# Kernel tuning notes

Hardware: AMD Instinct MI355X
Metric: run time of the kernel (lower is better)

The kernel has to match this reference:

```python
import jax, jax.numpy as jnp
import numpy as np

D = 1024
H = 16
DH = D // H


def setup_inputs() -> dict:
    key = jax.random.key(0)
    ks = jax.random.split(key, 11)
    B, T = 4, 2048
    s = 0.02
    return {
        "q": jax.random.normal(ks[0], (B, T, D), jnp.float32),
        "k": jax.random.normal(ks[1], (B, T, D), jnp.float32),
        "v": jax.random.normal(ks[2], (B, T, D), jnp.float32),
        "Wq": jax.random.normal(ks[3], (D, D), jnp.float32) * s,
        "b_q": jax.random.normal(ks[4], (D,), jnp.float32) * s,
        "Wk": jax.random.normal(ks[5], (D, D), jnp.float32) * s,
        "b_k": jax.random.normal(ks[6], (D,), jnp.float32) * s,
        "Wv": jax.random.normal(ks[7], (D, D), jnp.float32) * s,
        "b_v": jax.random.normal(ks[8], (D,), jnp.float32) * s,
        "Wo": jax.random.normal(ks[9], (D, D), jnp.float32) * s,
        "b_o": jax.random.normal(ks[10], (D,), jnp.float32) * s,
    }


def reference(q, k, v, Wq, b_q, Wk, b_k, Wv, b_v, Wo, b_o):
    B, Tq, _ = q.shape
    Tk = k.shape[1]
    # linear projections, split heads: [B,T,H,DH]
    Q = (q @ Wq + b_q).reshape(B, Tq, H, DH)
    K = (k @ Wk + b_k).reshape(B, Tk, H, DH)
    V = (v @ Wv + b_v).reshape(B, Tk, H, DH)
    # scaled dot-product attention (scale by sqrt(dh), matching q.shape[-1])
    scores = jnp.einsum('bthd,bshd->bhts', Q, K) / jnp.sqrt(jnp.float32(DH))
    P = jax.nn.softmax(scores, axis=-1)  # [B,H,Tq,Tk]
    out = jnp.einsum('bhts,bshd->bthd', P, V).reshape(B, Tq, D)
    return out @ Wo + b_o
```

## Files before the change

kernel.cpp:

```cpp
#include <hip/hip_runtime.h>
#include <hip/hip_bf16.h>


typedef __attribute__((ext_vector_type(8))) short bf16x8;
typedef __attribute__((ext_vector_type(4))) float f32x4;
typedef __attribute__((ext_vector_type(16))) float f32x16;

constexpr int Bc  = 4;
constexpr int Tc  = 2048;
constexpr int Dc  = 1024;
constexpr int Hc  = 16;
constexpr int DHc = 64;
constexpr int Mc  = Bc * Tc;

#define DI __device__ __forceinline__
#define MFMA32 __builtin_amdgcn_mfma_f32_32x32x16_bf16

DI void gload_lds16(const void* g, void* lds) {
  __builtin_amdgcn_global_load_lds((const __attribute__((address_space(1))) void*)g,
                                   (__attribute__((address_space(3))) void*)lds, 16, 0, 0);
}

DI uint pkbf(float lo, float hi) {
  union { __hip_bfloat16 h[2]; uint u; } t;
  t.h[0] = __float2bfloat16(lo);
  t.h[1] = __float2bfloat16(hi);
  return t.u;
}

DI f32x16 zero16() {
  f32x16 z;
#pragma unroll
  for (int i = 0; i < 16; ++i) z[i] = 0.f;
  return z;
}

__global__ __launch_bounds__(256) void cvt_f32_bf16(const float* __restrict__ in,
                                                    __hip_bfloat16* __restrict__ out,
                                                    int n8) {
  int i = blockIdx.x * 256 + threadIdx.x;
  if (i >= n8) return;
  float4 a = ((const float4*)in)[(size_t)i * 2];
  float4 b = ((const float4*)in)[(size_t)i * 2 + 1];
  alignas(16) __hip_bfloat16 t[8];
  t[0] = __float2bfloat16(a.x); t[1] = __float2bfloat16(a.y);
  t[2] = __float2bfloat16(a.z); t[3] = __float2bfloat16(a.w);
  t[4] = __float2bfloat16(b.x); t[5] = __float2bfloat16(b.y);
  t[6] = __float2bfloat16(b.z); t[7] = __float2bfloat16(b.w);
  *(uint4*)(out + (size_t)i * 8) = *(const uint4*)t;
}

__global__ __launch_bounds__(256) void wtrans(const float* __restrict__ W,
                                              __hip_bfloat16* __restrict__ Wt) {
  __shared__ __hip_bfloat16 tile[32][33];
  int n0 = blockIdx.x * 32, k0 = blockIdx.y * 32;
  int tx = threadIdx.x, ty = threadIdx.y;
#pragma unroll
  for (int i = 0; i < 4; ++i) {
    int k = ty + i * 8;
    tile[k][tx] = __float2bfloat16(W[(size_t)(k0 + k) * Dc + n0 + tx]);
  }
  __syncthreads();
#pragma unroll
  for (int i = 0; i < 4; ++i) {
    int n = ty + i * 8;
    Wt[(size_t)(n0 + n) * Dc + k0 + tx] = tile[tx][n];
  }
}

__global__ __launch_bounds__(256) void vtrans(const __hip_bfloat16* __restrict__ Vn,
                                              __hip_bfloat16* __restrict__ Vt) {
  __shared__ __hip_bfloat16 tile[64][72];
  int t0 = blockIdx.x * 64, h = blockIdx.y, b = blockIdx.z;
  int tid = threadIdx.x;
  int r = tid >> 3, ch = tid & 7;
#pragma unroll
  for (int half = 0; half < 2; ++half) {
    int row = r + half * 32;
    *(bf16x8*)&tile[row][ch * 8] =
        *(const bf16x8*)(Vn + ((size_t)(b * Tc + t0 + row)) * Dc + h * DHc + ch * 8);
  }
  __syncthreads();
#pragma unroll
  for (int half = 0; half < 2; ++half) {
    int dh = r + half * 32;
    bf16x8 v;
#pragma unroll
    for (int j = 0; j < 8; ++j) v[j] = *(const short*)&tile[ch * 8 + j][dh];
    *(bf16x8*)(Vt + ((size_t)((b * Hc + h) * DHc + dh)) * Tc + t0 + ch * 8) = v;
  }
}

template <bool OUT_BF16>
__global__ __launch_bounds__(256) void gemm_bt(const __hip_bfloat16* __restrict__ A,
                                               const __hip_bfloat16* __restrict__ Bt,
                                               const float* __restrict__ bias,
                                               void* __restrict__ Cout,
                                               int M, int N, int Kd, float scale) {
  constexpr int BK = 32;
  __shared__ __hip_bfloat16 Alds[128][BK];
  __shared__ __hip_bfloat16 Blds[128][BK];
  int tid = threadIdx.x;
  int w = tid >> 6, l = tid & 63;
  int lr = l & 15, lh = l >> 4;
  int wr = w >> 1, wc = w & 1;

  int g = blockIdx.y * gridDim.x + blockIdx.x;
  int nwg = gridDim.x * gridDim.y;
  int swz = ((g & 7) * (nwg >> 3)) + (g >> 3);
  int nbx = gridDim.x;
  int bx = swz % nbx, by = swz / nbx;
  int brow = by * 128, bcol = bx * 128;

  f32x4 acc[4][4];
#pragma unroll
  for (int mi = 0; mi < 4; ++mi)
#pragma unroll
    for (int ni = 0; ni < 4; ++ni) acc[mi][ni] = (f32x4){0.f, 0.f, 0.f, 0.f};

  int srow_in_ch = l >> 2;
  int scol = (l & 3) * 8;

  const int nkt = Kd / BK;
  for (int kt = 0; kt < nkt; ++kt) {
#pragma unroll
    for (int c = 0; c < 2; ++c) {
      int wch = w * 2 + c;
      int row = wch * 16 + srow_in_ch;
      const __hip_bfloat16* ga = A  + ((size_t)(brow + row)) * Kd + kt * BK + scol;
      const __hip_bfloat16* gb = Bt + ((size_t)(bcol + row)) * Kd + kt * BK + scol;
      gload_lds16(ga, (char*)&Alds[0][0] + wch * 1024);
      gload_lds16(gb, (char*)&Blds[0][0] + wch * 1024);
    }
    __syncthreads();
    bf16x8 af[4], bfr[4];
#pragma unroll
    for (int mi = 0; mi < 4; ++mi)
      af[mi] = *(const bf16x8*)&Alds[wr * 64 + mi * 16 + lr][lh * 8];
#pragma unroll
    for (int ni = 0; ni < 4; ++ni)
      bfr[ni] = *(const bf16x8*)&Blds[wc * 64 + ni * 16 + lr][lh * 8];
#pragma unroll
    for (int mi = 0; mi < 4; ++mi)
#pragma unroll
      for (int ni = 0; ni < 4; ++ni)
        acc[mi][ni] = __builtin_amdgcn_mfma_f32_16x16x32_bf16(af[mi], bfr[ni], acc[mi][ni], 0, 0, 0);
    __syncthreads();
  }

#pragma unroll
  for (int mi = 0; mi < 4; ++mi)
#pragma unroll
    for (int ni = 0; ni < 4; ++ni) {
      int row = brow + wr * 64 + mi * 16 + lh * 4;
      int col = bcol + wc * 64 + ni * 16 + lr;
      float bv = bias[col];
#pragma unroll
      for (int i = 0; i < 4; ++i) {
        float v = (acc[mi][ni][i] + bv) * scale;
        if (OUT_BF16)
          ((__hip_bfloat16*)Cout)[(size_t)(row + i) * N + col] = __float2bfloat16(v);
        else
          ((float*)Cout)[(size_t)(row + i) * N + col] = v;
      }
    }
}

__global__ __launch_bounds__(256, 2) void attn(const __hip_bfloat16* __restrict__ Q,
                                               const __hip_bfloat16* __restrict__ K,
                                               const __hip_bfloat16* __restrict__ Vt,
                                               __hip_bfloat16* __restrict__ O) {
  __shared__ __hip_bfloat16 Kl[2][64][64];
  __shared__ __hip_bfloat16 Vl[2][64][64];

  int g = blockIdx.x;
  int swz = (g & 7) * 128 + (g >> 3);
  int qt = swz & 15, h = (swz >> 4) & 15, b = swz >> 8;

  int tid = threadIdx.x, w = tid >> 6, l = tid & 63;
  int lane31 = l & 31, hi = l >> 5;
  int s7 = lane31 & 7;

  const __hip_bfloat16* qp =
      Q + ((size_t)(b * Tc + qt * 128 + w * 32 + lane31)) * Dc + h * DHc;
  bf16x8 qa[4];
#pragma unroll
  for (int c = 0; c < 4; ++c) qa[c] = *(const bf16x8*)(qp + c * 16 + hi * 8);

  int srow0 = w * 8 + (l >> 3);
  int srow1 = srow0 + 32;
  int sch0 = (l & 7) ^ (srow0 & 7);
  int sch1 = (l & 7) ^ (srow1 & 7);
  const __hip_bfloat16* kg0 = K + ((size_t)(b * Tc + srow0)) * Dc + h * DHc + sch0 * 8;
  const __hip_bfloat16* kg1 = K + ((size_t)(b * Tc + srow1)) * Dc + h * DHc + sch1 * 8;
  const __hip_bfloat16* vg0 = Vt + ((size_t)((b * Hc + h) * DHc + srow0)) * Tc + sch0 * 8;
  const __hip_bfloat16* vg1 = Vt + ((size_t)((b * Hc + h) * DHc + srow1)) * Tc + sch1 * 8;

  f32x16 o0 = zero16(), o1 = zero16();
  float lrun = 0.f;

  auto stage = [&](int buf) {
    char* kl = (char*)Kl + buf * 8192 + w * 1024;
    char* vl = (char*)Vl + buf * 8192 + w * 1024;
    gload_lds16(kg0, kl);
    gload_lds16(kg1, kl + 4096);
    gload_lds16(vg0, vl);
    gload_lds16(vg1, vl + 4096);
    kg0 += 64 * Dc; kg1 += 64 * Dc;
    vg0 += 64;      vg1 += 64;
  };

  auto compute = [&](int buf) {
    const __hip_bfloat16* Kb = &Kl[0][0][0] + buf * 4096;
    const __hip_bfloat16* Vb = &Vl[0][0][0] + buf * 4096;
    f32x16 s0 = zero16(), s1 = zero16();
    __builtin_amdgcn_s_setprio(1);
#pragma unroll
    for (int c = 0; c < 4; ++c) {
      int sl = ((2 * c + hi) ^ s7) * 8;
      bf16x8 k0 = *(const bf16x8*)(Kb + lane31 * 64 + sl);
      bf16x8 k1 = *(const bf16x8*)(Kb + 2048 + lane31 * 64 + sl);
      s0 = MFMA32(k0, qa[c], s0, 0, 0, 0);
      s1 = MFMA32(k1, qa[c], s1, 0, 0, 0);
    }
    __builtin_amdgcn_s_setprio(0);

#pragma unroll
    for (int i = 0; i < 16; ++i) s0[i] = __builtin_amdgcn_exp2f(s0[i]);
#pragma unroll
    for (int i = 0; i < 16; ++i) s1[i] = __builtin_amdgcn_exp2f(s1[i]);
    float rA = 0.f, rB = 0.f, rC = 0.f, rD = 0.f;
#pragma unroll
    for (int i = 0; i < 4; ++i) {
      rA += s0[i];      rB += s0[4 + i];
      rC += s0[8 + i];  rD += s0[12 + i];
      rA += s1[i];      rB += s1[4 + i];
      rC += s1[8 + i];  rD += s1[12 + i];
    }
    lrun += (rA + rB) + (rC + rD);

    __builtin_amdgcn_s_setprio(1);
#pragma unroll
    for (int cp = 0; cp < 4; ++cp) {
      const int bb = (cp & 1) * 8;
      const f32x16& sv = (cp >> 1) ? s1 : s0;
      uint x0 = pkbf(sv[bb + 0], sv[bb + 1]);
      uint x1 = pkbf(sv[bb + 2], sv[bb + 3]);
      uint y0 = pkbf(sv[bb + 4], sv[bb + 5]);
      uint y1 = pkbf(sv[bb + 6], sv[bb + 7]);
      auto w0 = __builtin_amdgcn_permlane32_swap(x0, y0, false, false);
      auto w1 = __builtin_amdgcn_permlane32_swap(x1, y1, false, false);
      union { uint u[4]; bf16x8 v; } pa;
      pa.u[0] = w0[0]; pa.u[1] = w1[0]; pa.u[2] = w0[1]; pa.u[3] = w1[1];
      int sl = ((2 * cp + hi) ^ s7) * 8;
      bf16x8 v0 = *(const bf16x8*)(Vb + lane31 * 64 + sl);
      bf16x8 v1 = *(const bf16x8*)(Vb + 2048 + lane31 * 64 + sl);
      o0 = MFMA32(pa.v, v0, o0, 0, 0, 0);
      o1 = MFMA32(pa.v, v1, o1, 0, 0, 0);
    }
    __builtin_amdgcn_s_setprio(0);
  };

  stage(0);
  __syncthreads();
  for (int kt = 0; kt < Tc / 64; kt += 2) {
    stage(1);
    compute(0);
    __syncthreads();
    if (kt + 2 < Tc / 64) stage(0);
    compute(1);
    __syncthreads();
  }

  lrun += __shfl_xor(lrun, 32);
  __hip_bfloat16* ob =
      O + ((size_t)(b * Tc + qt * 128 + w * 32)) * Dc + h * DHc + lane31;
#pragma unroll
  for (int r = 0; r < 16; ++r) {
    int qloc = (r & 3) + 8 * (r >> 2) + 4 * hi;
    float linv = __builtin_amdgcn_rcpf(__shfl(lrun, qloc));
    ob[(size_t)qloc * Dc]      = __float2bfloat16(o0[r] * linv);
    ob[(size_t)qloc * Dc + 32] = __float2bfloat16(o1[r] * linv);
  }
}

extern "C" void kernel_launch(void* const* d_in, const int* in_sizes, int n_in,
                              void* d_out, int out_size, void* d_ws, size_t ws_size,
                              hipStream_t stream) {
  const float* q  = (const float*)d_in[0];
  const float* k  = (const float*)d_in[1];
  const float* v  = (const float*)d_in[2];
  const float* Wq = (const float*)d_in[3];
  const float* bq = (const float*)d_in[4];
  const float* Wk = (const float*)d_in[5];
  const float* bk = (const float*)d_in[6];
  const float* Wv = (const float*)d_in[7];
  const float* bv = (const float*)d_in[8];
  const float* Wo = (const float*)d_in[9];
  const float* bo = (const float*)d_in[10];

  char* ws = (char*)d_ws;
  const size_t SZ = (size_t)Mc * Dc * 2;
  __hip_bfloat16* qb  = (__hip_bfloat16*)(ws + 0 * SZ);
  __hip_bfloat16* kb  = (__hip_bfloat16*)(ws + 1 * SZ);
  __hip_bfloat16* vb  = (__hip_bfloat16*)(ws + 2 * SZ);
  __hip_bfloat16* Qp  = (__hip_bfloat16*)(ws + 3 * SZ);
  __hip_bfloat16* Kp  = (__hip_bfloat16*)(ws + 4 * SZ);
  __hip_bfloat16* Vn  = (__hip_bfloat16*)(ws + 5 * SZ);
  __hip_bfloat16* WqT = (__hip_bfloat16*)(ws + 6 * SZ);
  __hip_bfloat16* WkT = WqT + (size_t)Dc * Dc;
  __hip_bfloat16* WvT = WkT + (size_t)Dc * Dc;
  __hip_bfloat16* WoT = WvT + (size_t)Dc * Dc;
  __hip_bfloat16* Vt    = kb;
  __hip_bfloat16* attnO = qb;

  const int n8 = Mc * Dc / 8;
  cvt_f32_bf16<<<n8 / 256, 256, 0, stream>>>(q, qb, n8);
  cvt_f32_bf16<<<n8 / 256, 256, 0, stream>>>(k, kb, n8);
  cvt_f32_bf16<<<n8 / 256, 256, 0, stream>>>(v, vb, n8);

  dim3 wgrid(Dc / 32, Dc / 32), wblk(32, 8);
  wtrans<<<wgrid, wblk, 0, stream>>>(Wq, WqT);
  wtrans<<<wgrid, wblk, 0, stream>>>(Wk, WkT);
  wtrans<<<wgrid, wblk, 0, stream>>>(Wv, WvT);
  wtrans<<<wgrid, wblk, 0, stream>>>(Wo, WoT);

  dim3 ggrid(Dc / 128, Mc / 128);
  gemm_bt<true><<<ggrid, 256, 0, stream>>>(qb, WqT, bq, Qp, Mc, Dc, Dc, 0.125f * 1.44269504f);
  gemm_bt<true><<<ggrid, 256, 0, stream>>>(kb, WkT, bk, Kp, Mc, Dc, Dc, 1.0f);
  gemm_bt<true><<<ggrid, 256, 0, stream>>>(vb, WvT, bv, Vn, Mc, Dc, Dc, 1.0f);

  vtrans<<<dim3(Tc / 64, Hc, Bc), 256, 0, stream>>>(Vn, Vt);

  attn<<<dim3(Tc / 128 * Hc * Bc), 256, 0, stream>>>(Qp, Kp, Vt, attnO);

  gemm_bt<false><<<ggrid, 256, 0, stream>>>(attnO, WoT, bo, (float*)d_out, Mc, Dc, Dc, 1.0f);
}
```

Before: 378.1 us.

## Double-buffer GEMM and attention loads, fuse launches, write V transposed in epilogue

```diff
diff --git a/kernel.cpp b/kernel.cpp
--- a/kernel.cpp
+++ b/kernel.cpp
@@ -16,6 +16,16 @@
 #define DI __device__ __forceinline__
 #define MFMA32 __builtin_amdgcn_mfma_f32_32x32x16_bf16
 
+#define FENCE() asm volatile("" ::: "memory")
+#define BAR()                                   \
+  do {                                          \
+    FENCE();                                    \
+    __builtin_amdgcn_s_barrier();               \
+    FENCE();                                    \
+    __builtin_amdgcn_sched_barrier(0);          \
+  } while (0)
+#define VMCNT(n) asm volatile("s_waitcnt vmcnt(" #n ")" ::: "memory")
+
 DI void gload_lds16(const void* g, void* lds) {
   __builtin_amdgcn_global_load_lds((const __attribute__((address_space(1))) void*)g,
                                    (__attribute__((address_space(3))) void*)lds, 16, 0, 0);
@@ -35,24 +45,35 @@
   return z;
 }
 
-__global__ __launch_bounds__(256) void cvt_f32_bf16(const float* __restrict__ in,
-                                                    __hip_bfloat16* __restrict__ out,
-                                                    int n8) {
-  int i = blockIdx.x * 256 + threadIdx.x;
-  if (i >= n8) return;
-  float4 a = ((const float4*)in)[(size_t)i * 2];
-  float4 b = ((const float4*)in)[(size_t)i * 2 + 1];
+__global__ __launch_bounds__(256) void cvt3(const float* __restrict__ q,
+                                            const float* __restrict__ k,
+                                            const float* __restrict__ v,
+                                            __hip_bfloat16* __restrict__ qb,
+                                            __hip_bfloat16* __restrict__ kb,
+                                            __hip_bfloat16* __restrict__ vb) {
+  int z = blockIdx.y;
+  const float* in = (z == 0) ? q : (z == 1) ? k : v;
+  __hip_bfloat16* out = (z == 0) ? qb : (z == 1) ? kb : vb;
+  size_t i = (size_t)blockIdx.x * 256 + threadIdx.x;
+  float4 a = ((const float4*)in)[i * 2];
+  float4 b = ((const float4*)in)[i * 2 + 1];
   alignas(16) __hip_bfloat16 t[8];
   t[0] = __float2bfloat16(a.x); t[1] = __float2bfloat16(a.y);
   t[2] = __float2bfloat16(a.z); t[3] = __float2bfloat16(a.w);
   t[4] = __float2bfloat16(b.x); t[5] = __float2bfloat16(b.y);
   t[6] = __float2bfloat16(b.z); t[7] = __float2bfloat16(b.w);
-  *(uint4*)(out + (size_t)i * 8) = *(const uint4*)t;
-}
-
-__global__ __launch_bounds__(256) void wtrans(const float* __restrict__ W,
-                                              __hip_bfloat16* __restrict__ Wt) {
+  *(uint4*)(out + i * 8) = *(const uint4*)t;
+}
+
+__global__ __launch_bounds__(256) void wtrans4(const float* __restrict__ Wq,
+                                               const float* __restrict__ Wk,
+                                               const float* __restrict__ Wv,
+                                               const float* __restrict__ Wo,
+                                               __hip_bfloat16* __restrict__ WT) {
   __shared__ __hip_bfloat16 tile[32][33];
+  int z = blockIdx.z;
+  const float* W = (z == 0) ? Wq : (z == 1) ? Wk : (z == 2) ? Wv : Wo;
+  __hip_bfloat16* Wt = WT + (size_t)z * Dc * Dc;
   int n0 = blockIdx.x * 32, k0 = blockIdx.y * 32;
   int tx = threadIdx.x, ty = threadIdx.y;
 #pragma unroll
@@ -68,38 +89,15 @@
   }
 }
 
-__global__ __launch_bounds__(256) void vtrans(const __hip_bfloat16* __restrict__ Vn,
-                                              __hip_bfloat16* __restrict__ Vt) {
-  __shared__ __hip_bfloat16 tile[64][72];
-  int t0 = blockIdx.x * 64, h = blockIdx.y, b = blockIdx.z;
-  int tid = threadIdx.x;
-  int r = tid >> 3, ch = tid & 7;
-#pragma unroll
-  for (int half = 0; half < 2; ++half) {
-    int row = r + half * 32;
-    *(bf16x8*)&tile[row][ch * 8] =
-        *(const bf16x8*)(Vn + ((size_t)(b * Tc + t0 + row)) * Dc + h * DHc + ch * 8);
-  }
-  __syncthreads();
-#pragma unroll
-  for (int half = 0; half < 2; ++half) {
-    int dh = r + half * 32;
-    bf16x8 v;
-#pragma unroll
-    for (int j = 0; j < 8; ++j) v[j] = *(const short*)&tile[ch * 8 + j][dh];
-    *(bf16x8*)(Vt + ((size_t)((b * Hc + h) * DHc + dh)) * Tc + t0 + ch * 8) = v;
-  }
-}
-
-template <bool OUT_BF16>
-__global__ __launch_bounds__(256) void gemm_bt(const __hip_bfloat16* __restrict__ A,
-                                               const __hip_bfloat16* __restrict__ Bt,
-                                               const float* __restrict__ bias,
-                                               void* __restrict__ Cout,
-                                               int M, int N, int Kd, float scale) {
+template <int OMODE>
+DI void gemm_body(const __hip_bfloat16* __restrict__ A,
+                  const __hip_bfloat16* __restrict__ Bt,
+                  const float* __restrict__ bias, void* __restrict__ Cout,
+                  float scale) {
   constexpr int BK = 32;
-  __shared__ __hip_bfloat16 Alds[128][BK];
-  __shared__ __hip_bfloat16 Blds[128][BK];
+  __shared__ __hip_bfloat16 Alds[2][128][BK];
+  __shared__ __hip_bfloat16 Blds[2][128][BK];
+  const int Kd = Dc, N = Dc;
   int tid = threadIdx.x;
   int w = tid >> 6, l = tid & 63;
   int lr = l & 15, lh = l >> 4;
@@ -108,8 +106,7 @@
   int g = blockIdx.y * gridDim.x + blockIdx.x;
   int nwg = gridDim.x * gridDim.y;
   int swz = ((g & 7) * (nwg >> 3)) + (g >> 3);
-  int nbx = gridDim.x;
-  int bx = swz % nbx, by = swz / nbx;
+  int bx = swz % gridDim.x, by = swz / gridDim.x;
   int brow = by * 128, bcol = bx * 128;
 
   f32x4 acc[4][4];
@@ -118,35 +115,50 @@
 #pragma unroll
     for (int ni = 0; ni < 4; ++ni) acc[mi][ni] = (f32x4){0.f, 0.f, 0.f, 0.f};
 
-  int srow_in_ch = l >> 2;
+  int srow = l >> 2;
   int scol = (l & 3) * 8;
-
-  const int nkt = Kd / BK;
-  for (int kt = 0; kt < nkt; ++kt) {
-#pragma unroll
-    for (int c = 0; c < 2; ++c) {
-      int wch = w * 2 + c;
-      int row = wch * 16 + srow_in_ch;
-      const __hip_bfloat16* ga = A  + ((size_t)(brow + row)) * Kd + kt * BK + scol;
-      const __hip_bfloat16* gb = Bt + ((size_t)(bcol + row)) * Kd + kt * BK + scol;
-      gload_lds16(ga, (char*)&Alds[0][0] + wch * 1024);
-      gload_lds16(gb, (char*)&Blds[0][0] + wch * 1024);
-    }
-    __syncthreads();
+  int row0 = w * 32 + srow, row1 = row0 + 16;
+  const __hip_bfloat16* ga0 = A  + (size_t)(brow + row0) * Kd + scol;
+  const __hip_bfloat16* ga1 = A  + (size_t)(brow + row1) * Kd + scol;
+  const __hip_bfloat16* gb0 = Bt + (size_t)(bcol + row0) * Kd + scol;
+  const __hip_bfloat16* gb1 = Bt + (size_t)(bcol + row1) * Kd + scol;
+
+  auto stage = [&](int buf) {
+    char* ab = (char*)Alds + buf * 8192;
+    char* bb = (char*)Blds + buf * 8192;
+    gload_lds16(ga0, ab + (w * 2) * 1024);
+    gload_lds16(ga1, ab + (w * 2 + 1) * 1024);
+    gload_lds16(gb0, bb + (w * 2) * 1024);
+    gload_lds16(gb1, bb + (w * 2 + 1) * 1024);
+    ga0 += BK; ga1 += BK; gb0 += BK; gb1 += BK;
+  };
+  auto compute = [&](int buf) {
     bf16x8 af[4], bfr[4];
 #pragma unroll
     for (int mi = 0; mi < 4; ++mi)
-      af[mi] = *(const bf16x8*)&Alds[wr * 64 + mi * 16 + lr][lh * 8];
+      af[mi] = *(const bf16x8*)&Alds[buf][wr * 64 + mi * 16 + lr][lh * 8];
 #pragma unroll
     for (int ni = 0; ni < 4; ++ni)
-      bfr[ni] = *(const bf16x8*)&Blds[wc * 64 + ni * 16 + lr][lh * 8];
+      bfr[ni] = *(const bf16x8*)&Blds[buf][wc * 64 + ni * 16 + lr][lh * 8];
 #pragma unroll
     for (int mi = 0; mi < 4; ++mi)
 #pragma unroll
       for (int ni = 0; ni < 4; ++ni)
         acc[mi][ni] = __builtin_amdgcn_mfma_f32_16x16x32_bf16(af[mi], bfr[ni], acc[mi][ni], 0, 0, 0);
-    __syncthreads();
-  }
+  };
+
+  const int nkt = Kd / BK;
+  stage(0);
+  for (int kt = 0; kt < nkt - 1; ++kt) {
+    stage((kt + 1) & 1);
+    VMCNT(4);
+    BAR();
+    compute(kt & 1);
+    BAR();
+  }
+  VMCNT(0);
+  BAR();
+  compute((nkt - 1) & 1);
 
 #pragma unroll
   for (int mi = 0; mi < 4; ++mi)
@@ -155,15 +167,52 @@
       int row = brow + wr * 64 + mi * 16 + lh * 4;
       int col = bcol + wc * 64 + ni * 16 + lr;
       float bv = bias[col];
-#pragma unroll
-      for (int i = 0; i < 4; ++i) {
-        float v = (acc[mi][ni][i] + bv) * scale;
-        if (OUT_BF16)
-          ((__hip_bfloat16*)Cout)[(size_t)(row + i) * N + col] = __float2bfloat16(v);
-        else
-          ((float*)Cout)[(size_t)(row + i) * N + col] = v;
+      if (OMODE == 2) {
+        union { __hip_bfloat16 h[4]; uint2 v2; } p;
+#pragma unroll
+        for (int i = 0; i < 4; ++i)
+          p.h[i] = __float2bfloat16(acc[mi][ni][i] + bv);
+        int b_ = row >> 11, t = row & 2047;
+        int h_ = col >> 6, dh = col & 63;
+        *(uint2*)((__hip_bfloat16*)Cout +
+                  (((size_t)(b_ * Hc + h_) * DHc + dh) * Tc + t)) = p.v2;
+      } else {
+#pragma unroll
+        for (int i = 0; i < 4; ++i) {
+          float v = (acc[mi][ni][i] + bv) * scale;
+          if (OMODE == 1)
+            ((__hip_bfloat16*)Cout)[(size_t)(row + i) * N + col] = __float2bfloat16(v);
+          else
+            ((float*)Cout)[(size_t)(row + i) * N + col] = v;
+        }
       }
     }
+}
+
+__global__ __launch_bounds__(256) void gemm_qk(const __hip_bfloat16* __restrict__ qb,
+                                               const __hip_bfloat16* __restrict__ kb,
+                                               const __hip_bfloat16* __restrict__ WqT,
+                                               const __hip_bfloat16* __restrict__ WkT,
+                                               const float* __restrict__ bq,
+                                               const float* __restrict__ bk,
+                                               __hip_bfloat16* __restrict__ Qp,
+                                               __hip_bfloat16* __restrict__ Kp,
+                                               float qscale) {
+  int z = blockIdx.z;
+  const __hip_bfloat16* A  = z ? kb : qb;
+  const __hip_bfloat16* Bt = z ? WkT : WqT;
+  const float* bias = z ? bk : bq;
+  __hip_bfloat16* C = z ? Kp : Qp;
+  float sc = z ? 1.0f : qscale;
+  gemm_body<1>(A, Bt, bias, C, sc);
+}
+
+template <int OMODE>
+__global__ __launch_bounds__(256) void gemm_one(const __hip_bfloat16* __restrict__ A,
+                                                const __hip_bfloat16* __restrict__ Bt,
+                                                const float* __restrict__ bias,
+                                                void* __restrict__ Cout, float scale) {
+  gemm_body<OMODE>(A, Bt, bias, Cout, scale);
 }
 
 __global__ __launch_bounds__(256, 2) void attn(const __hip_bfloat16* __restrict__ Q,
@@ -261,16 +310,18 @@
     __builtin_amdgcn_s_setprio(0);
   };
 
+  const int NT = Tc / 64;
   stage(0);
-  __syncthreads();
-  for (int kt = 0; kt < Tc / 64; kt += 2) {
-    stage(1);
-    compute(0);
-    __syncthreads();
-    if (kt + 2 < Tc / 64) stage(0);
-    compute(1);
-    __syncthreads();
-  }
+  for (int kt = 0; kt < NT - 1; ++kt) {
+    stage((kt + 1) & 1);
+    VMCNT(4);
+    BAR();
+    compute(kt & 1);
+    BAR();
+  }
+  VMCNT(0);
+  BAR();
+  compute((NT - 1) & 1);
 
   lrun += __shfl_xor(lrun, 32);
   __hip_bfloat16* ob =
@@ -306,33 +357,23 @@
   __hip_bfloat16* vb  = (__hip_bfloat16*)(ws + 2 * SZ);
   __hip_bfloat16* Qp  = (__hip_bfloat16*)(ws + 3 * SZ);
   __hip_bfloat16* Kp  = (__hip_bfloat16*)(ws + 4 * SZ);
-  __hip_bfloat16* Vn  = (__hip_bfloat16*)(ws + 5 * SZ);
-  __hip_bfloat16* WqT = (__hip_bfloat16*)(ws + 6 * SZ);
-  __hip_bfloat16* WkT = WqT + (size_t)Dc * Dc;
-  __hip_bfloat16* WvT = WkT + (size_t)Dc * Dc;
-  __hip_bfloat16* WoT = WvT + (size_t)Dc * Dc;
+  __hip_bfloat16* WT  = (__hip_bfloat16*)(ws + 5 * SZ);
+  __hip_bfloat16* WqT = WT;
+  __hip_bfloat16* WkT = WT + 1 * (size_t)Dc * Dc;
+  __hip_bfloat16* WvT = WT + 2 * (size_t)Dc * Dc;
+  __hip_bfloat16* WoT = WT + 3 * (size_t)Dc * Dc;
   __hip_bfloat16* Vt    = kb;
   __hip_bfloat16* attnO = qb;
 
-  const int n8 = Mc * Dc / 8;
-  cvt_f32_bf16<<<n8 / 256, 256, 0, stream>>>(q, qb, n8);
-  cvt_f32_bf16<<<n8 / 256, 256, 0, stream>>>(k, kb, n8);
-  cvt_f32_bf16<<<n8 / 256, 256, 0, stream>>>(v, vb, n8);
-
-  dim3 wgrid(Dc / 32, Dc / 32), wblk(32, 8);
-  wtrans<<<wgrid, wblk, 0, stream>>>(Wq, WqT);
-  wtrans<<<wgrid, wblk, 0, stream>>>(Wk, WkT);
-  wtrans<<<wgrid, wblk, 0, stream>>>(Wv, WvT);
-  wtrans<<<wgrid, wblk, 0, stream>>>(Wo, WoT);
+  cvt3<<<dim3(Mc * Dc / 8 / 256, 3), 256, 0, stream>>>(q, k, v, qb, kb, vb);
+  wtrans4<<<dim3(Dc / 32, Dc / 32, 4), dim3(32, 8), 0, stream>>>(Wq, Wk, Wv, Wo, WT);
 
   dim3 ggrid(Dc / 128, Mc / 128);
-  gemm_bt<true><<<ggrid, 256, 0, stream>>>(qb, WqT, bq, Qp, Mc, Dc, Dc, 0.125f * 1.44269504f);
-  gemm_bt<true><<<ggrid, 256, 0, stream>>>(kb, WkT, bk, Kp, Mc, Dc, Dc, 1.0f);
-  gemm_bt<true><<<ggrid, 256, 0, stream>>>(vb, WvT, bv, Vn, Mc, Dc, Dc, 1.0f);
-
-  vtrans<<<dim3(Tc / 64, Hc, Bc), 256, 0, stream>>>(Vn, Vt);
+  gemm_qk<<<dim3(Dc / 128, Mc / 128, 2), 256, 0, stream>>>(
+      qb, kb, WqT, WkT, bq, bk, Qp, Kp, 0.125f * 1.44269504f);
+  gemm_one<2><<<ggrid, 256, 0, stream>>>(vb, WvT, bv, Vt, 1.0f);
 
   attn<<<dim3(Tc / 128 * Hc * Bc), 256, 0, stream>>>(Qp, Kp, Vt, attnO);
 
-  gemm_bt<false><<<ggrid, 256, 0, stream>>>(attnO, WoT, bo, (float*)d_out, Mc, Dc, Dc, 1.0f);
-}
+  gemm_one<0><<<ggrid, 256, 0, stream>>>(attnO, WoT, bo, (float*)d_out, 1.0f);
+}
```

After: 371.9 us. About the same (-1.6%).
